# Kernel tuning notes

Hardware: AMD Instinct MI355X
Metric: run time of the kernel (lower is better)

## Reference

```python
import jax, jax.numpy as jnp
import numpy as np

N, H = 768, 128
EPS_LN = 1e-5


def setup_inputs() -> dict:
    key = jax.random.key(0)
    ks = jax.random.split(key, 24)
    s = 0.02
    inp = {
        "node_features": jax.random.normal(ks[0], (N, H), jnp.float32),
        "vector_features": jax.random.normal(ks[1], (N, 3), jnp.float32),
        "positions": jax.random.normal(ks[2], (N, 3), jnp.float32) * 10.0,
        "pair_mask": jax.random.randint(ks[3], (N, N), 0, 2) > 0,
        "conservation_scores": jax.random.uniform(ks[4], (N, 1), jnp.float32),
        "membrane_mask": jnp.round(jax.random.uniform(ks[5], (N,), jnp.float32)),
        "catalytic_mask": jnp.round(jax.random.uniform(ks[6], (N,), jnp.float32)),
        # edge_mlp: Linear(2H+6 -> H), SiLU, Linear(H -> H)
        "eW1": jax.random.normal(ks[7], (2 * H + 6, H), jnp.float32) * s,
        "eb1": jnp.zeros((H,), jnp.float32),
        "eW2": jax.random.normal(ks[8], (H, H), jnp.float32) * s,
        "eb2": jnp.zeros((H,), jnp.float32),
        # scalar_update: Linear(2H -> H), SiLU, Linear(H -> H)
        "sW1": jax.random.normal(ks[9], (2 * H, H), jnp.float32) * s,
        "sb1": jnp.zeros((H,), jnp.float32),
        "sW2": jax.random.normal(ks[10], (H, H), jnp.float32) * s,
        "sb2": jnp.zeros((H,), jnp.float32),
        # vector_gate: Linear(H -> H), SiLU, Linear(H -> 1)
        "gW1": jax.random.normal(ks[11], (H, H), jnp.float32) * s,
        "gb1": jnp.zeros((H,), jnp.float32),
        "gW2": jax.random.normal(ks[12], (H, 1), jnp.float32) * s,
        "gb2": jnp.zeros((1,), jnp.float32),
        # LayerNorm(H)
        "ln_g": jnp.ones((H,), jnp.float32),
        "ln_b": jnp.zeros((H,), jnp.float32),
    }
    return inp


def reference(node_features, vector_features, positions, pair_mask,
              conservation_scores, membrane_mask, catalytic_mask,
              eW1, eb1, eW2, eb2, sW1, sb1, sW2, sb2,
              gW1, gb1, gW2, gb2, ln_g, ln_b):
    n = node_features.shape[0]
    dt = node_features.dtype

    rel = positions[:, None, :] - positions[None, :, :]          # [N,N,3]
    dist = jnp.maximum(jnp.linalg.norm(rel, axis=-1, keepdims=True), 1e-8)  # [N,N,1]
    direction = rel / dist                                        # [N,N,3]

    pm = pair_mask.astype(dt)                                     # [N,N]
    fi = jnp.broadcast_to(node_features[:, None, :], (n, n, node_features.shape[1]))
    fj = jnp.broadcast_to(node_features[None, :, :], (n, n, node_features.shape[1]))
    cons_i = jnp.broadcast_to(conservation_scores[:, None, :], (n, n, 1))
    cons_j = jnp.broadcast_to(conservation_scores[None, :, :], (n, n, 1))
    mem_i = jnp.broadcast_to(membrane_mask[:, None, None], (n, n, 1)).astype(dt)
    cat_j = jnp.broadcast_to(catalytic_mask[None, :, None], (n, n, 1)).astype(dt)

    edge_input = jnp.concatenate(
        [fi, fj, dist, cons_i, cons_j, mem_i, cat_j, pm[..., None]], axis=-1)  # [N,N,2H+6]

    edge_hidden = jax.nn.silu(edge_input @ eW1 + eb1) @ eW2 + eb2  # [N,N,H]
    edge_weights = jax.nn.sigmoid(edge_hidden.mean(axis=-1)) * pm  # [N,N]

    message_scalar = jnp.einsum('ijh,ij->ih', edge_hidden, edge_weights)  # [N,H]

    su_in = jnp.concatenate([node_features, message_scalar], axis=-1)     # [N,2H]
    su = jax.nn.silu(su_in @ sW1 + sb1) @ sW2 + sb2
    x = node_features + su
    mu = x.mean(axis=-1, keepdims=True)
    var = x.var(axis=-1, keepdims=True)
    scalar_out = (x - mu) / jnp.sqrt(var + EPS_LN) * ln_g + ln_b          # [N,H]

    vg = (jax.nn.silu(edge_hidden @ gW1 + gb1) @ gW2 + gb2)[..., 0] * edge_weights  # [N,N]
    vector_message = jnp.einsum('ij,ijc->ic', vg, direction)              # [N,3]
    vector_out = vector_features + vector_message

    return scalar_out, vector_out, edge_weights
```

## Files before the change

kernel.cpp:

```cpp
#include <hip/hip_runtime.h>

#define NN 768
#define HH 128
#define TJ 32
#define NT (NN / TJ)
#define THREADS 512

typedef __bf16 bf16x8 __attribute__((ext_vector_type(8)));
typedef float f32x4 __attribute__((ext_vector_type(4)));

union U8 { __bf16 h[8]; unsigned short s[8]; uint4 u; bf16x8 b; };
union U4 { __bf16 h[4]; uint2 u2; };

__device__ __forceinline__ float fast_sig(float x) {
    return __builtin_amdgcn_rcpf(1.0f + __expf(-x));
}
__device__ __forceinline__ float fast_silu(float x) { return x * fast_sig(x); }

__device__ __forceinline__ f32x4 MFMA(bf16x8 a, bf16x8 b, f32x4 c) {
    return __builtin_amdgcn_mfma_f32_16x16x32_bf16(a, b, c, 0, 0, 0);
}

__device__ __forceinline__ bf16x8 ldfrag(const unsigned short* buf, int off) {
    U8 r;
    r.u = *(const uint4*)((const char*)buf + off);
    return r.b;
}

__global__ void precompute_proj(const float* __restrict__ nf,
                                const float* __restrict__ cons,
                                const float* __restrict__ memb,
                                const float* __restrict__ cata,
                                const float* __restrict__ eW1,
                                const float* __restrict__ eb1,
                                float* __restrict__ AiP,
                                float* __restrict__ AjP) {
    __shared__ float row[HH];
    int i = blockIdx.x;
    int h = threadIdx.x;
    row[h] = nf[i * HH + h];
    __syncthreads();
    float ci = cons[i], mi = memb[i], ti = cata[i];
    float ai = eb1[h] + ci * eW1[257 * HH + h] + mi * eW1[259 * HH + h];
    float aj = ci * eW1[258 * HH + h] + ti * eW1[260 * HH + h];
    for (int k = 0; k < HH; ++k) {
        float x = row[k];
        ai = fmaf(x, eW1[k * HH + h], ai);
        aj = fmaf(x, eW1[(HH + k) * HH + h], aj);
    }
    AiP[i * HH + h] = ai;
    AjP[i * HH + h] = aj;
}

__global__ void __launch_bounds__(THREADS, 4)
main_kernel(const float* __restrict__ nf, const float* __restrict__ vf,
            const float* __restrict__ pos, const int* __restrict__ pm,
            const float* __restrict__ eW1, const float* __restrict__ eW2,
            const float* __restrict__ eb2,
            const float* __restrict__ sW1, const float* __restrict__ sb1,
            const float* __restrict__ sW2, const float* __restrict__ sb2,
            const float* __restrict__ gW1, const float* __restrict__ gb1,
            const float* __restrict__ gW2, const float* __restrict__ gb2,
            const float* __restrict__ ln_g, const float* __restrict__ ln_b,
            const float* __restrict__ AiP, const float* __restrict__ AjP,
            float* __restrict__ out_scalar, float* __restrict__ out_vec,
            float* __restrict__ out_ew) {
    __shared__ __align__(16) unsigned short S1[TJ * HH];
    __shared__ __align__(16) unsigned short EH[TJ * HH];
    __shared__ float distL[NN];
    __shared__ float dirxL[NN], diryL[NN], dirzL[NN];
    __shared__ float pmvL[NN];
    __shared__ __align__(16) float baseI[HH];
    __shared__ __align__(16) float wdR[HH];
    __shared__ __align__(16) float wpR[HH];
    __shared__ __align__(16) float ebL[HH];
    __shared__ __align__(16) float gbL[HH];
    __shared__ __align__(16) float g2L[HH];
    __shared__ __align__(16) float ewL[TJ];
    __shared__ float ewpart[8][33];
    __shared__ float vpart[TJ][9];
    __shared__ __align__(16) float mpart[HH];
    __shared__ float vbuf[TJ * 3];
    __shared__ float suin[2 * HH];
    __shared__ float hbuf[HH];
    __shared__ float red2[4];

    const int t = threadIdx.x;
    const int i = blockIdx.x;

    {
        const float pxi = pos[i * 3 + 0], pyi = pos[i * 3 + 1], pzi = pos[i * 3 + 2];
        for (int j = t; j < NN; j += THREADS) {
            float rx = pxi - pos[j * 3 + 0];
            float ry = pyi - pos[j * 3 + 1];
            float rz = pzi - pos[j * 3 + 2];
            float d = sqrtf(rx * rx + ry * ry + rz * rz);
            d = fmaxf(d, 1e-8f);
            float inv = 1.0f / d;
            distL[j] = d;
            dirxL[j] = rx * inv;
            diryL[j] = ry * inv;
            dirzL[j] = rz * inv;
            pmvL[j] = (pm[i * NN + j] != 0) ? 1.0f : 0.0f;
        }
        if (t < HH) {
            baseI[t] = AiP[i * HH + t];
            wdR[t] = eW1[256 * HH + t];
            wpR[t] = eW1[261 * HH + t];
            ebL[t] = eb2[t];
            gbL[t] = gb1[t];
            g2L[t] = gW2[t];
        }
    }

    const int w = t >> 6, l = t & 63;
    const int lr = l & 15;
    const int lg = l >> 4;
    const int colxor = (lr & 15) << 4;
    const int aoff0 = lr * 256 + ((  0 + lg * 16) ^ colxor);
    const int aoff1 = lr * 256 + (( 64 + lg * 16) ^ colxor);
    const int aoff2 = lr * 256 + ((128 + lg * 16) ^ colxor);
    const int aoff3 = lr * 256 + ((192 + lg * 16) ^ colxor);
    const int ewr0 = lr * 256 + (((w * 32 + lg * 8)) ^ colxor);
    const int ewr1 = ewr0 + 4096;
    const int hq = w * 16 + lg * 4;

    auto loadA = [&](const float* __restrict__ W, int kc) -> bf16x8 {
        U8 tmp;
        int col = w * 16 + lr;
#pragma unroll
        for (int e = 0; e < 8; ++e)
            tmp.h[e] = (__bf16)W[(kc * 32 + lg * 8 + e) * HH + col];
        asm volatile("" : "+v"(tmp.u.x), "+v"(tmp.u.y),
                          "+v"(tmp.u.z), "+v"(tmp.u.w));
        return tmp.b;
    };
    const bf16x8 Wf0 = loadA(eW2, 0), Wf1 = loadA(eW2, 1),
                 Wf2 = loadA(eW2, 2), Wf3 = loadA(eW2, 3);
    const bf16x8 Gf0 = loadA(gW1, 0), Gf1 = loadA(gW1, 1),
                 Gf2 = loadA(gW1, 2), Gf3 = loadA(gW1, 3);

    const float gb2s = gb2[0];

    const int jj_s = t >> 4;
    const int h8 = (t & 15) * 8;
    const int s1woff = jj_s * 256 + (((t & 15) * 16) ^ ((jj_s & 15) << 4));

    float macc0 = 0.f, macc1 = 0.f, macc2 = 0.f, macc3 = 0.f;
    float vmx = 0.f, vmy = 0.f, vmz = 0.f;

    __syncthreads();

    for (int jt = 0; jt < NT; ++jt) {
        const int j0 = jt * TJ;

        {
            int j = j0 + jj_s;
            float4 bj0 = *(const float4*)&AjP[j * HH + h8];
            float4 bj1 = *(const float4*)&AjP[j * HH + h8 + 4];
            float4 a0 = *(const float4*)&baseI[h8];
            float4 a1 = *(const float4*)&baseI[h8 + 4];
            float4 w0 = *(const float4*)&wdR[h8];
            float4 w1 = *(const float4*)&wdR[h8 + 4];
            float4 p0 = *(const float4*)&wpR[h8];
            float4 p1 = *(const float4*)&wpR[h8 + 4];
            float d = distL[j], pf = pmvL[j];
            U8 pk;
            pk.h[0] = (__bf16)fast_silu(a0.x + bj0.x + d * w0.x + pf * p0.x);
            pk.h[1] = (__bf16)fast_silu(a0.y + bj0.y + d * w0.y + pf * p0.y);
            pk.h[2] = (__bf16)fast_silu(a0.z + bj0.z + d * w0.z + pf * p0.z);
            pk.h[3] = (__bf16)fast_silu(a0.w + bj0.w + d * w0.w + pf * p0.w);
            pk.h[4] = (__bf16)fast_silu(a1.x + bj1.x + d * w1.x + pf * p1.x);
            pk.h[5] = (__bf16)fast_silu(a1.y + bj1.y + d * w1.y + pf * p1.y);
            pk.h[6] = (__bf16)fast_silu(a1.z + bj1.z + d * w1.z + pf * p1.z);
            pk.h[7] = (__bf16)fast_silu(a1.w + bj1.w + d * w1.w + pf * p1.w);
            *(uint4*)((char*)S1 + s1woff) = pk.u;
        }
        __syncthreads();

        f32x4 acc0, acc1;
        {
            float4 eb4 = *(const float4*)&ebL[hq];
            acc0[0] = eb4.x; acc0[1] = eb4.y; acc0[2] = eb4.z; acc0[3] = eb4.w;
            acc1 = acc0;
        }
        {
            bf16x8 b;
            b = ldfrag(S1, aoff0);        acc0 = MFMA(Wf0, b, acc0);
            b = ldfrag(S1, aoff0 + 4096); acc1 = MFMA(Wf0, b, acc1);
            b = ldfrag(S1, aoff1);        acc0 = MFMA(Wf1, b, acc0);
            b = ldfrag(S1, aoff1 + 4096); acc1 = MFMA(Wf1, b, acc1);
            b = ldfrag(S1, aoff2);        acc0 = MFMA(Wf2, b, acc0);
            b = ldfrag(S1, aoff2 + 4096); acc1 = MFMA(Wf2, b, acc1);
            b = ldfrag(S1, aoff3);        acc0 = MFMA(Wf3, b, acc0);
            b = ldfrag(S1, aoff3 + 4096); acc1 = MFMA(Wf3, b, acc1);
        }

        {
            float s0 = acc0[0] + acc0[1] + acc0[2] + acc0[3];
            float s1 = acc1[0] + acc1[1] + acc1[2] + acc1[3];
            s0 += __shfl_xor(s0, 16); s0 += __shfl_xor(s0, 32);
            s1 += __shfl_xor(s1, 16); s1 += __shfl_xor(s1, 32);
            if (l < 16) {
                ewpart[w][l] = s0;
                ewpart[w][16 + l] = s1;
            }
        }
        {
            U4 p0, p1;
            p0.h[0] = (__bf16)acc0[0]; p0.h[1] = (__bf16)acc0[1];
            p0.h[2] = (__bf16)acc0[2]; p0.h[3] = (__bf16)acc0[3];
            p1.h[0] = (__bf16)acc1[0]; p1.h[1] = (__bf16)acc1[1];
            p1.h[2] = (__bf16)acc1[2]; p1.h[3] = (__bf16)acc1[3];
            *(uint2*)((char*)EH + ewr0) = p0.u2;
            *(uint2*)((char*)EH + ewr1) = p1.u2;
        }
        __syncthreads();

        if (l < 4) {
            int j = w * 4 + l;
            float s = ewpart[0][j] + ewpart[1][j] + ewpart[2][j] + ewpart[3][j]
                    + ewpart[4][j] + ewpart[5][j] + ewpart[6][j] + ewpart[7][j];
            float ewv = fast_sig(s * (1.0f / HH)) * pmvL[j0 + j];
            ewL[j] = ewv;
            out_ew[i * NN + j0 + j] = ewv;
        }
        f32x4 g0, g1;
        {
            float4 gb4 = *(const float4*)&gbL[hq];
            g0[0] = gb4.x; g0[1] = gb4.y; g0[2] = gb4.z; g0[3] = gb4.w;
            g1 = g0;
        }
        {
            bf16x8 b;
            b = ldfrag(EH, aoff0);        g0 = MFMA(Gf0, b, g0);
            b = ldfrag(EH, aoff0 + 4096); g1 = MFMA(Gf0, b, g1);
            b = ldfrag(EH, aoff1);        g0 = MFMA(Gf1, b, g0);
            b = ldfrag(EH, aoff1 + 4096); g1 = MFMA(Gf1, b, g1);
            b = ldfrag(EH, aoff2);        g0 = MFMA(Gf2, b, g0);
            b = ldfrag(EH, aoff2 + 4096); g1 = MFMA(Gf2, b, g1);
            b = ldfrag(EH, aoff3);        g0 = MFMA(Gf3, b, g0);
            b = ldfrag(EH, aoff3 + 4096); g1 = MFMA(Gf3, b, g1);
        }
        {
            float4 g2v = *(const float4*)&g2L[hq];
            float s0 = fast_silu(g0[0]) * g2v.x + fast_silu(g0[1]) * g2v.y
                     + fast_silu(g0[2]) * g2v.z + fast_silu(g0[3]) * g2v.w;
            float s1 = fast_silu(g1[0]) * g2v.x + fast_silu(g1[1]) * g2v.y
                     + fast_silu(g1[2]) * g2v.z + fast_silu(g1[3]) * g2v.w;
            s0 += __shfl_xor(s0, 16); s0 += __shfl_xor(s0, 32);
            s1 += __shfl_xor(s1, 16); s1 += __shfl_xor(s1, 32);
            if (l < 16) {
                vpart[l][w] = s0;
                vpart[16 + l][w] = s1;
            }
        }
        __syncthreads();

        {
            float e0 = ewL[lr], e1 = ewL[16 + lr];
            macc0 += e0 * acc0[0] + e1 * acc1[0];
            macc1 += e0 * acc0[1] + e1 * acc1[1];
            macc2 += e0 * acc0[2] + e1 * acc1[2];
            macc3 += e0 * acc0[3] + e1 * acc1[3];
        }
        if (l < 4) {
            int j = w * 4 + l;
            float s = vpart[j][0] + vpart[j][1] + vpart[j][2] + vpart[j][3]
                    + vpart[j][4] + vpart[j][5] + vpart[j][6] + vpart[j][7];
            float vg = (s + gb2s) * ewL[j];
            vmx = fmaf(vg, dirxL[j0 + j], vmx);
            vmy = fmaf(vg, diryL[j0 + j], vmy);
            vmz = fmaf(vg, dirzL[j0 + j], vmz);
        }
    }

    if (l < 4) {
        int j = w * 4 + l;
        vbuf[j * 3 + 0] = vmx;
        vbuf[j * 3 + 1] = vmy;
        vbuf[j * 3 + 2] = vmz;
    }
    macc0 += __shfl_xor(macc0, 1); macc0 += __shfl_xor(macc0, 2);
    macc0 += __shfl_xor(macc0, 4); macc0 += __shfl_xor(macc0, 8);
    macc1 += __shfl_xor(macc1, 1); macc1 += __shfl_xor(macc1, 2);
    macc1 += __shfl_xor(macc1, 4); macc1 += __shfl_xor(macc1, 8);
    macc2 += __shfl_xor(macc2, 1); macc2 += __shfl_xor(macc2, 2);
    macc2 += __shfl_xor(macc2, 4); macc2 += __shfl_xor(macc2, 8);
    macc3 += __shfl_xor(macc3, 1); macc3 += __shfl_xor(macc3, 2);
    macc3 += __shfl_xor(macc3, 4); macc3 += __shfl_xor(macc3, 8);
    if (lr == 0) {
        *(float4*)&mpart[hq] = make_float4(macc0, macc1, macc2, macc3);
    }
    __syncthreads();

    if (t < HH) {
        suin[t] = nf[i * HH + t];
        suin[HH + t] = mpart[t];
    }
    __syncthreads();
    if (t < HH) {
        float a = sb1[t];
        for (int k = 0; k < 2 * HH; ++k) a = fmaf(suin[k], sW1[k * HH + t], a);
        hbuf[t] = fast_silu(a);
    }
    __syncthreads();
    float x = 0.f, sx = 0.f, sq = 0.f;
    if (t < HH) {
        float a = sb2[t];
        for (int k = 0; k < HH; ++k) a = fmaf(hbuf[k], sW2[k * HH + t], a);
        x = nf[i * HH + t] + a;
        sx = x;
        sq = x * x;
    }
#pragma unroll
    for (int msk = 1; msk <= 32; msk <<= 1) {
        sx += __shfl_xor(sx, msk);
        sq += __shfl_xor(sq, msk);
    }
    if (t == 0)  { red2[0] = sx; red2[1] = sq; }
    if (t == 64) { red2[2] = sx; red2[3] = sq; }
    __syncthreads();
    if (t < HH) {
        float mean = (red2[0] + red2[2]) * (1.0f / HH);
        float var  = (red2[1] + red2[3]) * (1.0f / HH) - mean * mean;
        out_scalar[i * HH + t] =
            (x - mean) * rsqrtf(var + 1e-5f) * ln_g[t] + ln_b[t];
    }
    if (t < 3) {
        float v = vf[i * 3 + t];
        for (int g = 0; g < TJ; ++g) v += vbuf[g * 3 + t];
        out_vec[i * 3 + t] = v;
    }
}

extern "C" void kernel_launch(void* const* d_in, const int* in_sizes, int n_in,
                              void* d_out, int out_size, void* d_ws, size_t ws_size,
                              hipStream_t stream) {
    const float* nf   = (const float*)d_in[0];
    const float* vf   = (const float*)d_in[1];
    const float* pos  = (const float*)d_in[2];
    const int*   pm   = (const int*)d_in[3];
    const float* cons = (const float*)d_in[4];
    const float* memb = (const float*)d_in[5];
    const float* cata = (const float*)d_in[6];
    const float* eW1  = (const float*)d_in[7];
    const float* eb1  = (const float*)d_in[8];
    const float* eW2  = (const float*)d_in[9];
    const float* eb2  = (const float*)d_in[10];
    const float* sW1  = (const float*)d_in[11];
    const float* sb1  = (const float*)d_in[12];
    const float* sW2  = (const float*)d_in[13];
    const float* sb2  = (const float*)d_in[14];
    const float* gW1  = (const float*)d_in[15];
    const float* gb1  = (const float*)d_in[16];
    const float* gW2  = (const float*)d_in[17];
    const float* gb2  = (const float*)d_in[18];
    const float* lng  = (const float*)d_in[19];
    const float* lnb  = (const float*)d_in[20];

    float* out = (float*)d_out;
    float* out_scalar = out;
    float* out_vec    = out + NN * HH;
    float* out_ew     = out + NN * HH + NN * 3;

    float* AiP = (float*)d_ws;
    float* AjP = AiP + NN * HH;

    precompute_proj<<<NN, HH, 0, stream>>>(nf, cons, memb, cata, eW1, eb1, AiP, AjP);

    main_kernel<<<NN, THREADS, 0, stream>>>(
        nf, vf, pos, pm, eW1, eW2, eb2, sW1, sb1, sW2, sb2, gW1, gb1, gW2, gb2,
        lng, lnb, AiP, AjP, out_scalar, out_vec, out_ew);
}
```

Baseline: 119.2 us.

## Double j-tile width and defer vector-gate reduction to next iteration

Raises the j tile from 32 to 64 pairs, so each wave issues four independent MFMA chains per stage and there are half as many loop iterations and barriers. The edge-weight reduction is now computed redundantly per lane in registers instead of by a few lanes via shared memory. The vector-gate reduction from each tile is deferred into the next iteration after its first barrier, which drops one __syncthreads per tile. The cost is more accumulator registers, which may lower occupancy, and larger shared buffers.

```diff
diff --git a/kernel.cpp b/kernel.cpp
--- a/kernel.cpp
+++ b/kernel.cpp
@@ -2,7 +2,7 @@
 
 #define NN 768
 #define HH 128
-#define TJ 32
+#define TJ 64
 #define NT (NN / TJ)
 #define THREADS 512
 
@@ -76,8 +76,8 @@
     __shared__ __align__(16) float ebL[HH];
     __shared__ __align__(16) float gbL[HH];
     __shared__ __align__(16) float g2L[HH];
-    __shared__ __align__(16) float ewL[TJ];
-    __shared__ float ewpart[8][33];
+    __shared__ float ewpart[8][65];
+    __shared__ float ewG[TJ];
     __shared__ float vpart[TJ][9];
     __shared__ __align__(16) float mpart[HH];
     __shared__ float vbuf[TJ * 3];
@@ -116,13 +116,12 @@
     const int w = t >> 6, l = t & 63;
     const int lr = l & 15;
     const int lg = l >> 4;
-    const int colxor = (lr & 15) << 4;
+    const int colxor = lr << 4;
     const int aoff0 = lr * 256 + ((  0 + lg * 16) ^ colxor);
     const int aoff1 = lr * 256 + (( 64 + lg * 16) ^ colxor);
     const int aoff2 = lr * 256 + ((128 + lg * 16) ^ colxor);
     const int aoff3 = lr * 256 + ((192 + lg * 16) ^ colxor);
-    const int ewr0 = lr * 256 + (((w * 32 + lg * 8)) ^ colxor);
-    const int ewr1 = ewr0 + 4096;
+    const int ewr0 = lr * 256 + ((w * 32 + lg * 8) ^ colxor);
     const int hq = w * 16 + lg * 4;
 
     auto loadA = [&](const float* __restrict__ W, int kc) -> bf16x8 {
@@ -155,131 +154,189 @@
         const int j0 = jt * TJ;
 
         {
-            int j = j0 + jj_s;
-            float4 bj0 = *(const float4*)&AjP[j * HH + h8];
-            float4 bj1 = *(const float4*)&AjP[j * HH + h8 + 4];
             float4 a0 = *(const float4*)&baseI[h8];
             float4 a1 = *(const float4*)&baseI[h8 + 4];
             float4 w0 = *(const float4*)&wdR[h8];
             float4 w1 = *(const float4*)&wdR[h8 + 4];
             float4 p0 = *(const float4*)&wpR[h8];
             float4 p1 = *(const float4*)&wpR[h8 + 4];
-            float d = distL[j], pf = pmvL[j];
-            U8 pk;
-            pk.h[0] = (__bf16)fast_silu(a0.x + bj0.x + d * w0.x + pf * p0.x);
-            pk.h[1] = (__bf16)fast_silu(a0.y + bj0.y + d * w0.y + pf * p0.y);
-            pk.h[2] = (__bf16)fast_silu(a0.z + bj0.z + d * w0.z + pf * p0.z);
-            pk.h[3] = (__bf16)fast_silu(a0.w + bj0.w + d * w0.w + pf * p0.w);
-            pk.h[4] = (__bf16)fast_silu(a1.x + bj1.x + d * w1.x + pf * p1.x);
-            pk.h[5] = (__bf16)fast_silu(a1.y + bj1.y + d * w1.y + pf * p1.y);
-            pk.h[6] = (__bf16)fast_silu(a1.z + bj1.z + d * w1.z + pf * p1.z);
-            pk.h[7] = (__bf16)fast_silu(a1.w + bj1.w + d * w1.w + pf * p1.w);
-            *(uint4*)((char*)S1 + s1woff) = pk.u;
+#pragma unroll
+            for (int rr = 0; rr < 2; ++rr) {
+                int j = j0 + jj_s + rr * 32;
+                float4 bj0 = *(const float4*)&AjP[j * HH + h8];
+                float4 bj1 = *(const float4*)&AjP[j * HH + h8 + 4];
+                float d = distL[j], pf = pmvL[j];
+                U8 pk;
+                pk.h[0] = (__bf16)fast_silu(a0.x + bj0.x + d * w0.x + pf * p0.x);
+                pk.h[1] = (__bf16)fast_silu(a0.y + bj0.y + d * w0.y + pf * p0.y);
+                pk.h[2] = (__bf16)fast_silu(a0.z + bj0.z + d * w0.z + pf * p0.z);
+                pk.h[3] = (__bf16)fast_silu(a0.w + bj0.w + d * w0.w + pf * p0.w);
+                pk.h[4] = (__bf16)fast_silu(a1.x + bj1.x + d * w1.x + pf * p1.x);
+                pk.h[5] = (__bf16)fast_silu(a1.y + bj1.y + d * w1.y + pf * p1.y);
+                pk.h[6] = (__bf16)fast_silu(a1.z + bj1.z + d * w1.z + pf * p1.z);
+                pk.h[7] = (__bf16)fast_silu(a1.w + bj1.w + d * w1.w + pf * p1.w);
+                *(uint4*)((char*)S1 + s1woff + rr * 8192) = pk.u;
+            }
         }
         __syncthreads();
 
-        f32x4 acc0, acc1;
+        if (jt > 0 && l < 8) {
+            int jj = w * 8 + l;
+            int jp = j0 - TJ + jj;
+            float s = vpart[jj][0] + vpart[jj][1] + vpart[jj][2] + vpart[jj][3]
+                    + vpart[jj][4] + vpart[jj][5] + vpart[jj][6] + vpart[jj][7];
+            float vg = (s + gb2s) * ewG[jj];
+            vmx = fmaf(vg, dirxL[jp], vmx);
+            vmy = fmaf(vg, diryL[jp], vmy);
+            vmz = fmaf(vg, dirzL[jp], vmz);
+        }
+
+        f32x4 acc0, acc1, acc2, acc3;
         {
             float4 eb4 = *(const float4*)&ebL[hq];
             acc0[0] = eb4.x; acc0[1] = eb4.y; acc0[2] = eb4.z; acc0[3] = eb4.w;
-            acc1 = acc0;
+            acc1 = acc0; acc2 = acc0; acc3 = acc0;
         }
         {
             bf16x8 b;
-            b = ldfrag(S1, aoff0);        acc0 = MFMA(Wf0, b, acc0);
-            b = ldfrag(S1, aoff0 + 4096); acc1 = MFMA(Wf0, b, acc1);
-            b = ldfrag(S1, aoff1);        acc0 = MFMA(Wf1, b, acc0);
-            b = ldfrag(S1, aoff1 + 4096); acc1 = MFMA(Wf1, b, acc1);
-            b = ldfrag(S1, aoff2);        acc0 = MFMA(Wf2, b, acc0);
-            b = ldfrag(S1, aoff2 + 4096); acc1 = MFMA(Wf2, b, acc1);
-            b = ldfrag(S1, aoff3);        acc0 = MFMA(Wf3, b, acc0);
-            b = ldfrag(S1, aoff3 + 4096); acc1 = MFMA(Wf3, b, acc1);
-        }
-
+            b = ldfrag(S1, aoff0);         acc0 = MFMA(Wf0, b, acc0);
+            b = ldfrag(S1, aoff0 + 4096);  acc1 = MFMA(Wf0, b, acc1);
+            b = ldfrag(S1, aoff0 + 8192);  acc2 = MFMA(Wf0, b, acc2);
+            b = ldfrag(S1, aoff0 + 12288); acc3 = MFMA(Wf0, b, acc3);
+            b = ldfrag(S1, aoff1);         acc0 = MFMA(Wf1, b, acc0);
+            b = ldfrag(S1, aoff1 + 4096);  acc1 = MFMA(Wf1, b, acc1);
+            b = ldfrag(S1, aoff1 + 8192);  acc2 = MFMA(Wf1, b, acc2);
+            b = ldfrag(S1, aoff1 + 12288); acc3 = MFMA(Wf1, b, acc3);
+            b = ldfrag(S1, aoff2);         acc0 = MFMA(Wf2, b, acc0);
+            b = ldfrag(S1, aoff2 + 4096);  acc1 = MFMA(Wf2, b, acc1);
+            b = ldfrag(S1, aoff2 + 8192);  acc2 = MFMA(Wf2, b, acc2);
+            b = ldfrag(S1, aoff2 + 12288); acc3 = MFMA(Wf2, b, acc3);
+            b = ldfrag(S1, aoff3);         acc0 = MFMA(Wf3, b, acc0);
+            b = ldfrag(S1, aoff3 + 4096);  acc1 = MFMA(Wf3, b, acc1);
+            b = ldfrag(S1, aoff3 + 8192);  acc2 = MFMA(Wf3, b, acc2);
+            b = ldfrag(S1, aoff3 + 12288); acc3 = MFMA(Wf3, b, acc3);
+        }
         {
             float s0 = acc0[0] + acc0[1] + acc0[2] + acc0[3];
             float s1 = acc1[0] + acc1[1] + acc1[2] + acc1[3];
+            float s2 = acc2[0] + acc2[1] + acc2[2] + acc2[3];
+            float s3 = acc3[0] + acc3[1] + acc3[2] + acc3[3];
             s0 += __shfl_xor(s0, 16); s0 += __shfl_xor(s0, 32);
             s1 += __shfl_xor(s1, 16); s1 += __shfl_xor(s1, 32);
+            s2 += __shfl_xor(s2, 16); s2 += __shfl_xor(s2, 32);
+            s3 += __shfl_xor(s3, 16); s3 += __shfl_xor(s3, 32);
             if (l < 16) {
-                ewpart[w][l] = s0;
+                ewpart[w][l]      = s0;
                 ewpart[w][16 + l] = s1;
+                ewpart[w][32 + l] = s2;
+                ewpart[w][48 + l] = s3;
             }
         }
         {
-            U4 p0, p1;
+            U4 p0, p1, p2, p3;
             p0.h[0] = (__bf16)acc0[0]; p0.h[1] = (__bf16)acc0[1];
             p0.h[2] = (__bf16)acc0[2]; p0.h[3] = (__bf16)acc0[3];
             p1.h[0] = (__bf16)acc1[0]; p1.h[1] = (__bf16)acc1[1];
             p1.h[2] = (__bf16)acc1[2]; p1.h[3] = (__bf16)acc1[3];
-            *(uint2*)((char*)EH + ewr0) = p0.u2;
-            *(uint2*)((char*)EH + ewr1) = p1.u2;
+            p2.h[0] = (__bf16)acc2[0]; p2.h[1] = (__bf16)acc2[1];
+            p2.h[2] = (__bf16)acc2[2]; p2.h[3] = (__bf16)acc2[3];
+            p3.h[0] = (__bf16)acc3[0]; p3.h[1] = (__bf16)acc3[1];
+            p3.h[2] = (__bf16)acc3[2]; p3.h[3] = (__bf16)acc3[3];
+            *(uint2*)((char*)EH + ewr0)          = p0.u2;
+            *(uint2*)((char*)EH + ewr0 + 4096)   = p1.u2;
+            *(uint2*)((char*)EH + ewr0 + 8192)   = p2.u2;
+            *(uint2*)((char*)EH + ewr0 + 12288)  = p3.u2;
         }
         __syncthreads();
 
-        if (l < 4) {
-            int j = w * 4 + l;
-            float s = ewpart[0][j] + ewpart[1][j] + ewpart[2][j] + ewpart[3][j]
-                    + ewpart[4][j] + ewpart[5][j] + ewpart[6][j] + ewpart[7][j];
-            float ewv = fast_sig(s * (1.0f / HH)) * pmvL[j0 + j];
-            ewL[j] = ewv;
-            out_ew[i * NN + j0 + j] = ewv;
-        }
-        f32x4 g0, g1;
+        float ew0, ew1, ew2, ew3;
+        {
+            float s0 = 0.f, s1 = 0.f, s2 = 0.f, s3 = 0.f;
+#pragma unroll
+            for (int w2 = 0; w2 < 8; ++w2) {
+                s0 += ewpart[w2][lr];
+                s1 += ewpart[w2][16 + lr];
+                s2 += ewpart[w2][32 + lr];
+                s3 += ewpart[w2][48 + lr];
+            }
+            ew0 = fast_sig(s0 * (1.0f / HH)) * pmvL[j0 + lr];
+            ew1 = fast_sig(s1 * (1.0f / HH)) * pmvL[j0 + 16 + lr];
+            ew2 = fast_sig(s2 * (1.0f / HH)) * pmvL[j0 + 32 + lr];
+            ew3 = fast_sig(s3 * (1.0f / HH)) * pmvL[j0 + 48 + lr];
+        }
+        if (lg == 0 && (lr >> 3) == (w & 1)) {
+            int nt = w >> 1;
+            int jj = nt * 16 + lr;
+            float ewv = (nt == 0) ? ew0 : (nt == 1) ? ew1 : (nt == 2) ? ew2 : ew3;
+            out_ew[i * NN + j0 + jj] = ewv;
+            ewG[jj] = ewv;
+        }
+        macc0 += ew0 * acc0[0] + ew1 * acc1[0] + ew2 * acc2[0] + ew3 * acc3[0];
+        macc1 += ew0 * acc0[1] + ew1 * acc1[1] + ew2 * acc2[1] + ew3 * acc3[1];
+        macc2 += ew0 * acc0[2] + ew1 * acc1[2] + ew2 * acc2[2] + ew3 * acc3[2];
+        macc3 += ew0 * acc0[3] + ew1 * acc1[3] + ew2 * acc2[3] + ew3 * acc3[3];
+
+        f32x4 g0, g1, g2, g3;
         {
             float4 gb4 = *(const float4*)&gbL[hq];
             g0[0] = gb4.x; g0[1] = gb4.y; g0[2] = gb4.z; g0[3] = gb4.w;
-            g1 = g0;
+            g1 = g0; g2 = g0; g3 = g0;
         }
         {
             bf16x8 b;
-            b = ldfrag(EH, aoff0);        g0 = MFMA(Gf0, b, g0);
-            b = ldfrag(EH, aoff0 + 4096); g1 = MFMA(Gf0, b, g1);
-            b = ldfrag(EH, aoff1);        g0 = MFMA(Gf1, b, g0);
-            b = ldfrag(EH, aoff1 + 4096); g1 = MFMA(Gf1, b, g1);
-            b = ldfrag(EH, aoff2);        g0 = MFMA(Gf2, b, g0);
-            b = ldfrag(EH, aoff2 + 4096); g1 = MFMA(Gf2, b, g1);
-            b = ldfrag(EH, aoff3);        g0 = MFMA(Gf3, b, g0);
-            b = ldfrag(EH, aoff3 + 4096); g1 = MFMA(Gf3, b, g1);
+            b = ldfrag(EH, aoff0);         g0 = MFMA(Gf0, b, g0);
+            b = ldfrag(EH, aoff0 + 4096);  g1 = MFMA(Gf0, b, g1);
+            b = ldfrag(EH, aoff0 + 8192);  g2 = MFMA(Gf0, b, g2);
+            b = ldfrag(EH, aoff0 + 12288); g3 = MFMA(Gf0, b, g3);
+            b = ldfrag(EH, aoff1);         g0 = MFMA(Gf1, b, g0);
+            b = ldfrag(EH, aoff1 + 4096);  g1 = MFMA(Gf1, b, g1);
+            b = ldfrag(EH, aoff1 + 8192);  g2 = MFMA(Gf1, b, g2);
+            b = ldfrag(EH, aoff1 + 12288); g3 = MFMA(Gf1, b, g3);
+            b = ldfrag(EH, aoff2);         g0 = MFMA(Gf2, b, g0);
+            b = ldfrag(EH, aoff2 + 4096);  g1 = MFMA(Gf2, b, g1);
+            b = ldfrag(EH, aoff2 + 8192);  g2 = MFMA(Gf2, b, g2);
+            b = ldfrag(EH, aoff2 + 12288); g3 = MFMA(Gf2, b, g3);
+            b = ldfrag(EH, aoff3);         g0 = MFMA(Gf3, b, g0);
+            b = ldfrag(EH, aoff3 + 4096);  g1 = MFMA(Gf3, b, g1);
+            b = ldfrag(EH, aoff3 + 8192);  g2 = MFMA(Gf3, b, g2);
+            b = ldfrag(EH, aoff3 + 12288); g3 = MFMA(Gf3, b, g3);
         }
         {
             float4 g2v = *(const float4*)&g2L[hq];
-            float s0 = fast_silu(g0[0]) * g2v.x + fast_silu(g0[1]) * g2v.y
+            float v0 = fast_silu(g0[0]) * g2v.x + fast_silu(g0[1]) * g2v.y
                      + fast_silu(g0[2]) * g2v.z + fast_silu(g0[3]) * g2v.w;
-            float s1 = fast_silu(g1[0]) * g2v.x + fast_silu(g1[1]) * g2v.y
+            float v1 = fast_silu(g1[0]) * g2v.x + fast_silu(g1[1]) * g2v.y
                      + fast_silu(g1[2]) * g2v.z + fast_silu(g1[3]) * g2v.w;
-            s0 += __shfl_xor(s0, 16); s0 += __shfl_xor(s0, 32);
-            s1 += __shfl_xor(s1, 16); s1 += __shfl_xor(s1, 32);
+            float v2 = fast_silu(g2[0]) * g2v.x + fast_silu(g2[1]) * g2v.y
+                     + fast_silu(g2[2]) * g2v.z + fast_silu(g2[3]) * g2v.w;
+            float v3 = fast_silu(g3[0]) * g2v.x + fast_silu(g3[1]) * g2v.y
+                     + fast_silu(g3[2]) * g2v.z + fast_silu(g3[3]) * g2v.w;
+            v0 += __shfl_xor(v0, 16); v0 += __shfl_xor(v0, 32);
+            v1 += __shfl_xor(v1, 16); v1 += __shfl_xor(v1, 32);
+            v2 += __shfl_xor(v2, 16); v2 += __shfl_xor(v2, 32);
+            v3 += __shfl_xor(v3, 16); v3 += __shfl_xor(v3, 32);
             if (l < 16) {
-                vpart[l][w] = s0;
-                vpart[16 + l][w] = s1;
+                vpart[l][w]      = v0;
+                vpart[16 + l][w] = v1;
+                vpart[32 + l][w] = v2;
+                vpart[48 + l][w] = v3;
             }
         }
-        __syncthreads();
-
-        {
-            float e0 = ewL[lr], e1 = ewL[16 + lr];
-            macc0 += e0 * acc0[0] + e1 * acc1[0];
-            macc1 += e0 * acc0[1] + e1 * acc1[1];
-            macc2 += e0 * acc0[2] + e1 * acc1[2];
-            macc3 += e0 * acc0[3] + e1 * acc1[3];
-        }
-        if (l < 4) {
-            int j = w * 4 + l;
-            float s = vpart[j][0] + vpart[j][1] + vpart[j][2] + vpart[j][3]
-                    + vpart[j][4] + vpart[j][5] + vpart[j][6] + vpart[j][7];
-            float vg = (s + gb2s) * ewL[j];
-            vmx = fmaf(vg, dirxL[j0 + j], vmx);
-            vmy = fmaf(vg, diryL[j0 + j], vmy);
-            vmz = fmaf(vg, dirzL[j0 + j], vmz);
-        }
-    }
-
-    if (l < 4) {
-        int j = w * 4 + l;
-        vbuf[j * 3 + 0] = vmx;
-        vbuf[j * 3 + 1] = vmy;
-        vbuf[j * 3 + 2] = vmz;
+    }
+
+    __syncthreads();
+    if (l < 8) {
+        int jj = w * 8 + l;
+        int jp = (NT - 1) * TJ + jj;
+        float s = vpart[jj][0] + vpart[jj][1] + vpart[jj][2] + vpart[jj][3]
+                + vpart[jj][4] + vpart[jj][5] + vpart[jj][6] + vpart[jj][7];
+        float vg = (s + gb2s) * ewG[jj];
+        vmx = fmaf(vg, dirxL[jp], vmx);
+        vmy = fmaf(vg, diryL[jp], vmy);
+        vmz = fmaf(vg, dirzL[jp], vmz);
+        vbuf[jj * 3 + 0] = vmx;
+        vbuf[jj * 3 + 1] = vmy;
+        vbuf[jj * 3 + 2] = vmz;
     }
     macc0 += __shfl_xor(macc0, 1); macc0 += __shfl_xor(macc0, 2);
     macc0 += __shfl_xor(macc0, 4); macc0 += __shfl_xor(macc0, 8);
```

Result: faster. 109.1 us (-8.5%).
